# Optimization experiments

Measured on AMD Instinct MI355X. Metric: run time of the kernel, lower is better.

## Reference

```python
import jax, jax.numpy as jnp
import numpy as np

NU, NI, D, H = 200000, 100000, 128, 128
E = 600000

def _segment_mean(vals, seg_ids, num_segments):
    s = jax.ops.segment_sum(vals, seg_ids, num_segments=num_segments)
    cnt = jax.ops.segment_sum(jnp.ones((vals.shape[0],), vals.dtype), seg_ids, num_segments=num_segments)
    return s / jnp.maximum(cnt, 1.0)[:, None]


def setup_inputs() -> dict:
    key = jax.random.key(0)
    ks = jax.random.split(key, 16)
    sc = 1.0 / np.sqrt(D)
    return {
        'x_user': jax.random.normal(ks[0], (NU, D), jnp.float32),
        'x_item': jax.random.normal(ks[1], (NI, D), jnp.float32),
        'edge_src_ui': jax.random.randint(ks[2], (E,), 0, NU),
        'edge_dst_ui': jax.random.randint(ks[3], (E,), 0, NI),
        'edge_src_iu': jax.random.randint(ks[4], (E,), 0, NI),
        'edge_dst_iu': jax.random.randint(ks[5], (E,), 0, NU),
        'Wl_ui': jax.random.normal(ks[6], (D, H), jnp.float32) * sc,
        'bl_ui': jax.random.normal(ks[7], (H,), jnp.float32) * 0.01,
        'Wr_ui': jax.random.normal(ks[8], (D, H), jnp.float32) * sc,
        'Wl_iu': jax.random.normal(ks[9], (D, H), jnp.float32) * sc,
        'bl_iu': jax.random.normal(ks[10], (H,), jnp.float32) * 0.01,
        'Wr_iu': jax.random.normal(ks[11], (D, H), jnp.float32) * sc,
        'W_user': jax.random.normal(ks[12], (H, H), jnp.float32) * sc,
        'b_user': jax.random.normal(ks[13], (H,), jnp.float32) * 0.01,
        'W_item': jax.random.normal(ks[14], (H, H), jnp.float32) * sc,
        'b_item': jax.random.normal(ks[15], (H,), jnp.float32) * 0.01,
    }


def reference(x_user, x_item, edge_src_ui, edge_dst_ui, edge_src_iu, edge_dst_iu,
              Wl_ui, bl_ui, Wr_ui, Wl_iu, bl_iu, Wr_iu,
              W_user, b_user, W_item, b_item):
    # SAGEConv per edge type: out_dst = mean_aggr(x_src[src]) @ Wl + bl + x_dst @ Wr
    agg_item = _segment_mean(x_user[edge_src_ui], edge_dst_ui, NI)   # [NI, D]
    h_item = agg_item @ Wl_ui + bl_ui + x_item @ Wr_ui               # [NI, H]
    agg_user = _segment_mean(x_item[edge_src_iu], edge_dst_iu, NU)   # [NU, D]
    h_user = agg_user @ Wl_iu + bl_iu + x_user @ Wr_iu               # [NU, H]
    # HeteroConv aggr='sum' is trivial here (one edge type per dst node type).
    out_user = jax.nn.relu(h_user @ W_user + b_user)
    out_item = jax.nn.relu(h_item @ W_item + b_item)
    return jnp.concatenate([out_user, out_item], axis=0)  # [NU+NI, H]
```

## Files before the change

### kernel.cpp

```cpp
#include <hip/hip_runtime.h>

#define NUu 200000
#define NIi 100000
#define EE  600000

#define SCAP 1024
#define NB_USER 3125
#define NB_ITEM 1563

typedef short short8 __attribute__((ext_vector_type(8)));
typedef float floatx4 __attribute__((ext_vector_type(4)));

__device__ __forceinline__ unsigned short f2bf(float f) {
  union { float f; unsigned int u; } v; v.f = f;
  unsigned int r = v.u + 0x7FFFu + ((v.u >> 16) & 1u);
  return (unsigned short)(r >> 16);
}

__global__ __launch_bounds__(128) void fuse_weights(
    const float* __restrict__ Wl_iu, const float* __restrict__ Wr_iu,
    const float* __restrict__ Wl_ui, const float* __restrict__ Wr_ui,
    const float* __restrict__ W_user, const float* __restrict__ W_item,
    unsigned short* __restrict__ Wp_user, unsigned short* __restrict__ Wp_item)
{
  int d = blockIdx.x;
  int m = blockIdx.y;
  int h = threadIdx.x;
  const float* A; const float* W; unsigned short* dst; int koff;
  switch (m) {
    case 0:  A = Wl_iu; W = W_user; dst = Wp_user; koff = 0;   break;
    case 1:  A = Wr_iu; W = W_user; dst = Wp_user; koff = 128; break;
    case 2:  A = Wl_ui; W = W_item; dst = Wp_item; koff = 0;   break;
    default: A = Wr_ui; W = W_item; dst = Wp_item; koff = 128; break;
  }
  float acc = 0.f;
  for (int k = 0; k < 128; ++k) acc += A[d * 128 + k] * W[k * 128 + h];
  int kg = koff + d;
  int ks = kg >> 5, quad = (kg >> 3) & 3, j = kg & 7;
  int nt = h >> 4, nlo = h & 15;
  int idx = ((nt * 8 + ks) * 64 + quad * 16 + nlo) * 8 + j;
  dst[idx] = f2bf(acc);
}

__global__ __launch_bounds__(128) void fuse_bias(
    const float* __restrict__ bl_iu, const float* __restrict__ b_user, const float* __restrict__ Wu,
    const float* __restrict__ bl_ui, const float* __restrict__ b_item, const float* __restrict__ Wi,
    float* __restrict__ bias_user, float* __restrict__ bias_item)
{
  int h = threadIdx.x;
  const float* bl = blockIdx.x ? bl_ui : bl_iu;
  const float* b2 = blockIdx.x ? b_item : b_user;
  const float* W  = blockIdx.x ? Wi : Wu;
  float* o        = blockIdx.x ? bias_item : bias_user;
  float acc = b2[h];
  for (int k = 0; k < 128; ++k) acc += bl[k] * W[k * 128 + h];
  o[h] = acc;
}

__global__ __launch_bounds__(256) void hist2(
    const int* __restrict__ edst_iu, int* __restrict__ cnt_user,
    const int* __restrict__ edst_ui, int* __restrict__ cnt_item)
{
  int e = blockIdx.x * 256 + threadIdx.x;
  if (e >= EE) return;
  const int* edst = blockIdx.y ? edst_ui : edst_iu;
  int* cnt        = blockIdx.y ? cnt_item : cnt_user;
  atomicAdd(&cnt[edst[e]], 1);
}

__global__ __launch_bounds__(256) void scan1(
    const int* __restrict__ cnt_u, int* __restrict__ blk_u,
    const int* __restrict__ cnt_i, int* __restrict__ blk_i)
{
  __shared__ int s[256];
  int b = blockIdx.x, t = threadIdx.x;
  const int* cnt; int* blksum; int N;
  if (blockIdx.y == 0) { cnt = cnt_u; blksum = blk_u; N = NUu; }
  else { if (b >= 98) return; cnt = cnt_i; blksum = blk_i; N = NIi; }
  int base = b * 1024 + t * 4;
  int v = 0;
  #pragma unroll
  for (int j = 0; j < 4; ++j) { int i = base + j; if (i < N) v += cnt[i]; }
  s[t] = v; __syncthreads();
  for (int off = 128; off > 0; off >>= 1) {
    if (t < off) s[t] += s[t + off];
    __syncthreads();
  }
  if (t == 0) blksum[b] = s[0];
}

__global__ __launch_bounds__(256) void scan2(
    const int* __restrict__ bs_u, int* __restrict__ bo_u,
    const int* __restrict__ bs_i, int* __restrict__ bo_i)
{
  __shared__ int s[256];
  int t = threadIdx.x;
  const int* blksum = blockIdx.x ? bs_i : bs_u;
  int* blkoff       = blockIdx.x ? bo_i : bo_u;
  int nblk          = blockIdx.x ? 98 : 196;
  int v = t < nblk ? blksum[t] : 0;
  s[t] = v; __syncthreads();
  for (int off = 1; off < 256; off <<= 1) {
    int tmp = t >= off ? s[t - off] : 0;
    __syncthreads();
    s[t] += tmp;
    __syncthreads();
  }
  if (t < nblk) blkoff[t] = s[t] - v;
}

__global__ __launch_bounds__(256) void scan3(
    const int* __restrict__ cnt_u, const int* __restrict__ bo_u,
    int* __restrict__ row_u, int* __restrict__ fil_u,
    const int* __restrict__ cnt_i, const int* __restrict__ bo_i,
    int* __restrict__ row_i, int* __restrict__ fil_i)
{
  __shared__ int s[256];
  int b = blockIdx.x, t = threadIdx.x;
  const int* cnt; const int* blkoff; int* rowp; int* fillp; int N;
  if (blockIdx.y == 0) { cnt = cnt_u; blkoff = bo_u; rowp = row_u; fillp = fil_u; N = NUu; }
  else { if (b >= 98) return; cnt = cnt_i; blkoff = bo_i; rowp = row_i; fillp = fil_i; N = NIi; }
  int base = b * 1024 + t * 4;
  int v[4]; int sum = 0;
  #pragma unroll
  for (int j = 0; j < 4; ++j) { int i = base + j; v[j] = (i < N) ? cnt[i] : 0; sum += v[j]; }
  s[t] = sum; __syncthreads();
  for (int off = 1; off < 256; off <<= 1) {
    int tmp = t >= off ? s[t - off] : 0;
    __syncthreads();
    s[t] += tmp;
    __syncthreads();
  }
  int ex = s[t] - sum + blkoff[b];
  #pragma unroll
  for (int j = 0; j < 4; ++j) {
    int i = base + j;
    if (i < N) { rowp[i] = ex; fillp[i] = ex; ex += v[j]; }
  }
}

__global__ __launch_bounds__(256) void fill2(
    const int* __restrict__ esrc_iu, const int* __restrict__ edst_iu,
    int* __restrict__ fill_user, int* __restrict__ srcs_user,
    const int* __restrict__ esrc_ui, const int* __restrict__ edst_ui,
    int* __restrict__ fill_item, int* __restrict__ srcs_item)
{
  int e = blockIdx.x * 256 + threadIdx.x;
  if (e >= EE) return;
  const int* esrc; const int* edst; int* fillp; int* srcs;
  if (blockIdx.y == 0) { esrc = esrc_iu; edst = edst_iu; fillp = fill_user; srcs = srcs_user; }
  else                 { esrc = esrc_ui; edst = edst_ui; fillp = fill_item; srcs = srcs_item; }
  int d = edst[e];
  int p = atomicAdd(&fillp[d], 1);
  srcs[p] = esrc[e];
}

__global__ __launch_bounds__(256, 6) void fused_gemm(
    const float* __restrict__ xu_own, const float* __restrict__ xu_src,
    const int* __restrict__ rowp_u, const int* __restrict__ srcs_u,
    const unsigned short* __restrict__ Wp_u, const float* __restrict__ bias_u,
    const float* __restrict__ xi_own, const float* __restrict__ xi_src,
    const int* __restrict__ rowp_i, const int* __restrict__ srcs_i,
    const unsigned short* __restrict__ Wp_i, const float* __restrict__ bias_i,
    float* __restrict__ out)
{
  __shared__ __align__(16) uint4 ldsA4[1024];
  __shared__ int ldsS[SCAP];
  __shared__ int rb[65];
  int t = threadIdx.x;
  int b = blockIdx.x;

  const float* xown; const float* xsrc; const int* rowp; const int* srcs;
  const unsigned short* Wp; const float* bias; float* outbase; int nvalid; int node0;
  if (b < NB_USER) {
    xown = xu_own; xsrc = xu_src; rowp = rowp_u; srcs = srcs_u;
    Wp = Wp_u; bias = bias_u; outbase = out; nvalid = NUu; node0 = b * 64;
  } else {
    xown = xi_own; xsrc = xi_src; rowp = rowp_i; srcs = srcs_i;
    Wp = Wp_i; bias = bias_i; outbase = out + (size_t)NUu * 128;
    nvalid = NIi; node0 = (b - NB_USER) * 64;
  }

  if (t < 65) {
    int node = node0 + t;
    rb[t] = node < nvalid ? rowp[node] : EE;
  }
  __syncthreads();
  int rs0 = rb[0];
  int W = rb[64] - rs0;
  for (int idx = t; idx < W && idx < SCAP; idx += 256)
    ldsS[idx] = srcs[rs0 + idx];

  #pragma unroll
  for (int i = 0; i < 4; ++i) {
    int oid = t + i * 256;
    int m = oid >> 4;
    int oct = oid & 15;
    int node = node0 + m;
    uint4 p; p.x = 0u; p.y = 0u; p.z = 0u; p.w = 0u;
    if (node < nvalid) {
      const float4* p4 = (const float4*)(xown + (size_t)node * 128 + oct * 8);
      float4 lo = p4[0], hi = p4[1];
      p.x = (unsigned)f2bf(lo.x) | ((unsigned)f2bf(lo.y) << 16);
      p.y = (unsigned)f2bf(lo.z) | ((unsigned)f2bf(lo.w) << 16);
      p.z = (unsigned)f2bf(hi.x) | ((unsigned)f2bf(hi.y) << 16);
      p.w = (unsigned)f2bf(hi.z) | ((unsigned)f2bf(hi.w) << 16);
    }
    int ks = oct >> 2, quad = oct & 3;
    int mt = m >> 4, mlo = m & 15;
    ldsA4[(mt * 4 + ks) * 64 + quad * 16 + (mlo ^ (oct & 7))] = p;
  }
  __syncthreads();

  int wave = t >> 6, lane = t & 63;
  int quadr = lane >> 4, mlor = lane & 15;
  floatx4 acc[8];
  #pragma unroll
  for (int i = 0; i < 8; ++i) acc[i] = (floatx4){0.f, 0.f, 0.f, 0.f};
  const short8* A = (const short8*)ldsA4;
  const short8* B = (const short8*)Wp;
  #pragma unroll
  for (int kk = 0; kk < 4; ++kk) {
    short8 af = A[(wave * 4 + kk) * 64 + quadr * 16 + (mlor ^ ((kk * 4 + quadr) & 7))];
    #pragma unroll
    for (int nt = 0; nt < 8; ++nt) {
      short8 bf = B[(nt * 8 + 4 + kk) * 64 + lane];
      acc[nt] = __builtin_amdgcn_mfma_f32_16x16x32_bf16(af, bf, acc[nt], 0, 0, 0);
    }
  }
  __syncthreads();

  #pragma unroll
  for (int i = 0; i < 8; ++i) {
    int oid = t + i * 256;
    int m = oid >> 5;
    int oct = oid & 31;
    int slice = oct & 15;
    int par = oct >> 4;
    int node = node0 + m;
    float a0=0,a1=0,a2=0,a3=0,a4=0,a5=0,a6=0,a7=0;
    int deg = 0;
    if (node < nvalid) {
      int erel = rb[m] - rs0;
      deg = rb[m + 1] - rb[m];
      int k0 = slice * 8;
      int e = par;
      for (; e + 2 < deg; e += 4) {
        int q0 = erel + e, q1 = q0 + 2;
        int s0 = (q0 < SCAP) ? ldsS[q0] : srcs[rs0 + q0];
        int s1 = (q1 < SCAP) ? ldsS[q1] : srcs[rs0 + q1];
        const float4* r0 = (const float4*)(xsrc + (size_t)s0 * 128 + k0);
        const float4* r1 = (const float4*)(xsrc + (size_t)s1 * 128 + k0);
        float4 l0 = r0[0], h0 = r0[1];
        float4 l1 = r1[0], h1 = r1[1];
        a0 += l0.x + l1.x; a1 += l0.y + l1.y;
        a2 += l0.z + l1.z; a3 += l0.w + l1.w;
        a4 += h0.x + h1.x; a5 += h0.y + h1.y;
        a6 += h0.z + h1.z; a7 += h0.w + h1.w;
      }
      if (e < deg) {
        int q = erel + e;
        int s = (q < SCAP) ? ldsS[q] : srcs[rs0 + q];
        const float4* r = (const float4*)(xsrc + (size_t)s * 128 + k0);
        float4 l = r[0], h = r[1];
        a0 += l.x; a1 += l.y; a2 += l.z; a3 += l.w;
        a4 += h.x; a5 += h.y; a6 += h.z; a7 += h.w;
      }
    }
    a0 += __shfl_xor(a0, 16); a1 += __shfl_xor(a1, 16);
    a2 += __shfl_xor(a2, 16); a3 += __shfl_xor(a3, 16);
    a4 += __shfl_xor(a4, 16); a5 += __shfl_xor(a5, 16);
    a6 += __shfl_xor(a6, 16); a7 += __shfl_xor(a7, 16);
    if (par == 0) {
      float sc = deg > 0 ? 1.0f / (float)deg : 0.f;
      uint4 p;
      p.x = (unsigned)f2bf(a0 * sc) | ((unsigned)f2bf(a1 * sc) << 16);
      p.y = (unsigned)f2bf(a2 * sc) | ((unsigned)f2bf(a3 * sc) << 16);
      p.z = (unsigned)f2bf(a4 * sc) | ((unsigned)f2bf(a5 * sc) << 16);
      p.w = (unsigned)f2bf(a6 * sc) | ((unsigned)f2bf(a7 * sc) << 16);
      int ks = slice >> 2, quad = slice & 3;
      int mt = m >> 4, mlo = m & 15;
      ldsA4[(mt * 4 + ks) * 64 + quad * 16 + (mlo ^ (slice & 7))] = p;
    }
  }
  __syncthreads();

  #pragma unroll
  for (int kk = 0; kk < 4; ++kk) {
    short8 af = A[(wave * 4 + kk) * 64 + quadr * 16 + (mlor ^ ((kk * 4 + quadr) & 7))];
    #pragma unroll
    for (int nt = 0; nt < 8; ++nt) {
      short8 bf = B[(nt * 8 + kk) * 64 + lane];
      acc[nt] = __builtin_amdgcn_mfma_f32_16x16x32_bf16(af, bf, acc[nt], 0, 0, 0);
    }
  }

  int col = lane & 15, qrow = (lane >> 4) * 4;
  #pragma unroll
  for (int nt = 0; nt < 8; ++nt) {
    int n = nt * 16 + col;
    float bv = bias[n];
    #pragma unroll
    for (int r2 = 0; r2 < 4; ++r2) {
      int node = node0 + wave * 16 + qrow + r2;
      if (node < nvalid) {
        float v = acc[nt][r2] + bv;
        outbase[(size_t)node * 128 + n] = v > 0.f ? v : 0.f;
      }
    }
  }
}

extern "C" void kernel_launch(void* const* d_in, const int* in_sizes, int n_in,
                              void* d_out, int out_size, void* d_ws, size_t ws_size,
                              hipStream_t stream)
{
  const float* x_user = (const float*)d_in[0];
  const float* x_item = (const float*)d_in[1];
  const int* esrc_ui  = (const int*)d_in[2];
  const int* edst_ui  = (const int*)d_in[3];
  const int* esrc_iu  = (const int*)d_in[4];
  const int* edst_iu  = (const int*)d_in[5];
  const float* Wl_ui  = (const float*)d_in[6];
  const float* bl_ui  = (const float*)d_in[7];
  const float* Wr_ui  = (const float*)d_in[8];
  const float* Wl_iu  = (const float*)d_in[9];
  const float* bl_iu  = (const float*)d_in[10];
  const float* Wr_iu  = (const float*)d_in[11];
  const float* W_user = (const float*)d_in[12];
  const float* b_user = (const float*)d_in[13];
  const float* W_item = (const float*)d_in[14];
  const float* b_item = (const float*)d_in[15];
  float* out = (float*)d_out;

  char* ws = (char*)d_ws;
  int* cnt_user  = (int*)(ws + 0);
  int* cnt_item  = (int*)(ws + 800000);
  int* row_user  = (int*)(ws + 1200000);
  int* row_item  = (int*)(ws + 2000000);
  int* fill_user = (int*)(ws + 2400000);
  int* fill_item = (int*)(ws + 3200000);
  int* srcs_user = (int*)(ws + 3600000);
  int* srcs_item = (int*)(ws + 6000000);
  int* blks_user = (int*)(ws + 8400000);
  int* blks_item = (int*)(ws + 8401024);
  int* boff_user = (int*)(ws + 8402048);
  int* boff_item = (int*)(ws + 8403072);
  unsigned short* Wp_user = (unsigned short*)(ws + 8404224);
  unsigned short* Wp_item = (unsigned short*)(ws + 8469760);
  float* bias_user = (float*)(ws + 8535296);
  float* bias_item = (float*)(ws + 8535808);

  hipMemsetAsync(d_ws, 0, 1200000, stream);

  fuse_weights<<<dim3(128, 4), 128, 0, stream>>>(Wl_iu, Wr_iu, Wl_ui, Wr_ui,
                                                 W_user, W_item, Wp_user, Wp_item);
  fuse_bias<<<2, 128, 0, stream>>>(bl_iu, b_user, W_user, bl_ui, b_item, W_item,
                                   bias_user, bias_item);

  const int EB = (EE + 255) / 256;
  const int NBU = (NUu + 1023) / 1024;

  hist2<<<dim3(EB, 2), 256, 0, stream>>>(edst_iu, cnt_user, edst_ui, cnt_item);
  scan1<<<dim3(NBU, 2), 256, 0, stream>>>(cnt_user, blks_user, cnt_item, blks_item);
  scan2<<<2, 256, 0, stream>>>(blks_user, boff_user, blks_item, boff_item);
  scan3<<<dim3(NBU, 2), 256, 0, stream>>>(cnt_user, boff_user, row_user, fill_user,
                                          cnt_item, boff_item, row_item, fill_item);
  fill2<<<dim3(EB, 2), 256, 0, stream>>>(esrc_iu, edst_iu, fill_user, srcs_user,
                                         esrc_ui, edst_ui, fill_item, srcs_item);

  fused_gemm<<<NB_USER + NB_ITEM, 256, 0, stream>>>(
      x_user, x_item, row_user, srcs_user, Wp_user, bias_user,
      x_item, x_user, row_item, srcs_item, Wp_item, bias_item, out);
}
```

Before: 578.5 us.

## Pre-convert node features to bf16 and merge prep kernels into one launch

Adds a combined prep kernel that does the degree histogram (vectorized int4 loads), the weight and bias fusion, and a bf16 copy of x_user and x_item. The gather in fused_gemm can then read half-width rows when the workspace is large enough. The block-offset scan is folded into scan3, removing scan2. The change also raises launch bounds occupancy to 8, shrinks SCAP, and uses nontemporal output stores. The bf16 gather path lowers the precision of the aggregated sums and costs an extra full pass over the features to convert them. It only runs when ws_size is at least about 85 MB.

```diff
diff --git a/kernel.cpp b/kernel.cpp
--- a/kernel.cpp
+++ b/kernel.cpp
@@ -4,9 +4,16 @@
 #define NIi 100000
 #define EE  600000
 
-#define SCAP 1024
+#define SCAP 768
 #define NB_USER 3125
 #define NB_ITEM 1563
+
+#define PB_HIST   586
+#define PB_W0     1172
+#define PB_B0     1428
+#define PB_CU0    1429
+#define PB_CI0    13929
+#define PB_END    20179
 
 typedef short short8 __attribute__((ext_vector_type(8)));
 typedef float floatx4 __attribute__((ext_vector_type(4)));
@@ -16,56 +23,71 @@
   unsigned int r = v.u + 0x7FFFu + ((v.u >> 16) & 1u);
   return (unsigned short)(r >> 16);
 }
-
-__global__ __launch_bounds__(128) void fuse_weights(
+__device__ __forceinline__ float bflo(unsigned int u) { return __uint_as_float(u << 16); }
+__device__ __forceinline__ float bfhi(unsigned int u) { return __uint_as_float(u & 0xFFFF0000u); }
+
+__global__ __launch_bounds__(256) void prep(
+    const int* __restrict__ edst_iu, int* __restrict__ cnt_user,
+    const int* __restrict__ edst_ui, int* __restrict__ cnt_item,
     const float* __restrict__ Wl_iu, const float* __restrict__ Wr_iu,
     const float* __restrict__ Wl_ui, const float* __restrict__ Wr_ui,
     const float* __restrict__ W_user, const float* __restrict__ W_item,
-    unsigned short* __restrict__ Wp_user, unsigned short* __restrict__ Wp_item)
-{
-  int d = blockIdx.x;
-  int m = blockIdx.y;
-  int h = threadIdx.x;
-  const float* A; const float* W; unsigned short* dst; int koff;
-  switch (m) {
-    case 0:  A = Wl_iu; W = W_user; dst = Wp_user; koff = 0;   break;
-    case 1:  A = Wr_iu; W = W_user; dst = Wp_user; koff = 128; break;
-    case 2:  A = Wl_ui; W = W_item; dst = Wp_item; koff = 0;   break;
-    default: A = Wr_ui; W = W_item; dst = Wp_item; koff = 128; break;
-  }
-  float acc = 0.f;
-  for (int k = 0; k < 128; ++k) acc += A[d * 128 + k] * W[k * 128 + h];
-  int kg = koff + d;
-  int ks = kg >> 5, quad = (kg >> 3) & 3, j = kg & 7;
-  int nt = h >> 4, nlo = h & 15;
-  int idx = ((nt * 8 + ks) * 64 + quad * 16 + nlo) * 8 + j;
-  dst[idx] = f2bf(acc);
-}
-
-__global__ __launch_bounds__(128) void fuse_bias(
-    const float* __restrict__ bl_iu, const float* __restrict__ b_user, const float* __restrict__ Wu,
-    const float* __restrict__ bl_ui, const float* __restrict__ b_item, const float* __restrict__ Wi,
-    float* __restrict__ bias_user, float* __restrict__ bias_item)
-{
-  int h = threadIdx.x;
-  const float* bl = blockIdx.x ? bl_ui : bl_iu;
-  const float* b2 = blockIdx.x ? b_item : b_user;
-  const float* W  = blockIdx.x ? Wi : Wu;
-  float* o        = blockIdx.x ? bias_item : bias_user;
-  float acc = b2[h];
-  for (int k = 0; k < 128; ++k) acc += bl[k] * W[k * 128 + h];
-  o[h] = acc;
-}
-
-__global__ __launch_bounds__(256) void hist2(
-    const int* __restrict__ edst_iu, int* __restrict__ cnt_user,
-    const int* __restrict__ edst_ui, int* __restrict__ cnt_item)
-{
-  int e = blockIdx.x * 256 + threadIdx.x;
-  if (e >= EE) return;
-  const int* edst = blockIdx.y ? edst_ui : edst_iu;
-  int* cnt        = blockIdx.y ? cnt_item : cnt_user;
-  atomicAdd(&cnt[edst[e]], 1);
+    unsigned short* __restrict__ Wp_user, unsigned short* __restrict__ Wp_item,
+    const float* __restrict__ bl_iu, const float* __restrict__ b_user,
+    const float* __restrict__ bl_ui, const float* __restrict__ b_item,
+    float* __restrict__ bias_user, float* __restrict__ bias_item,
+    const float* __restrict__ x_user, const float* __restrict__ x_item,
+    unsigned short* __restrict__ xb_user, unsigned short* __restrict__ xb_item)
+{
+  int b = blockIdx.x, t = threadIdx.x;
+  if (b < PB_W0) {
+    const int* edst = b < PB_HIST ? edst_iu : edst_ui;
+    int* cnt        = b < PB_HIST ? cnt_user : cnt_item;
+    int local       = b < PB_HIST ? b : b - PB_HIST;
+    int idx = local * 1024 + t * 4;
+    if (idx < EE) {
+      int4 v = *(const int4*)(edst + idx);
+      atomicAdd(&cnt[v.x], 1); atomicAdd(&cnt[v.y], 1);
+      atomicAdd(&cnt[v.z], 1); atomicAdd(&cnt[v.w], 1);
+    }
+  } else if (b < PB_B0) {
+    int flat = (b - PB_W0) * 256 + t;
+    int h = flat & 127, d = (flat >> 7) & 127, m = flat >> 14;
+    const float* A; const float* W; unsigned short* dst; int koff;
+    switch (m) {
+      case 0:  A = Wl_iu; W = W_user; dst = Wp_user; koff = 0;   break;
+      case 1:  A = Wr_iu; W = W_user; dst = Wp_user; koff = 128; break;
+      case 2:  A = Wl_ui; W = W_item; dst = Wp_item; koff = 0;   break;
+      default: A = Wr_ui; W = W_item; dst = Wp_item; koff = 128; break;
+    }
+    float acc = 0.f;
+    for (int k = 0; k < 128; ++k) acc += A[d * 128 + k] * W[k * 128 + h];
+    int kg = koff + d;
+    int ks = kg >> 5, quad = (kg >> 3) & 3, j = kg & 7;
+    int nt = h >> 4, nlo = h & 15;
+    dst[((nt * 8 + ks) * 64 + quad * 16 + nlo) * 8 + j] = f2bf(acc);
+  } else if (b == PB_B0) {
+    int pair = t >> 7, h = t & 127;
+    const float* bl = pair ? bl_ui : bl_iu;
+    const float* b2 = pair ? b_item : b_user;
+    const float* W  = pair ? W_item : W_user;
+    float* o        = pair ? bias_item : bias_user;
+    float acc = b2[h];
+    for (int k = 0; k < 128; ++k) acc += bl[k] * W[k * 128 + h];
+    o[h] = acc;
+  } else {
+    const float* src; unsigned short* dst; long base;
+    if (b < PB_CI0) { src = x_user; dst = xb_user; base = (long)(b - PB_CU0) * 2048 + t * 8; }
+    else            { src = x_item; dst = xb_item; base = (long)(b - PB_CI0) * 2048 + t * 8; }
+    const float4* p4 = (const float4*)(src + base);
+    float4 lo = p4[0], hi = p4[1];
+    uint4 p;
+    p.x = (unsigned)f2bf(lo.x) | ((unsigned)f2bf(lo.y) << 16);
+    p.y = (unsigned)f2bf(lo.z) | ((unsigned)f2bf(lo.w) << 16);
+    p.z = (unsigned)f2bf(hi.x) | ((unsigned)f2bf(hi.y) << 16);
+    p.w = (unsigned)f2bf(hi.z) | ((unsigned)f2bf(hi.w) << 16);
+    *(uint4*)(dst + base) = p;
+  }
 }
 
 __global__ __launch_bounds__(256) void scan1(
@@ -89,37 +111,29 @@
   if (t == 0) blksum[b] = s[0];
 }
 
-__global__ __launch_bounds__(256) void scan2(
-    const int* __restrict__ bs_u, int* __restrict__ bo_u,
-    const int* __restrict__ bs_i, int* __restrict__ bo_i)
+__global__ __launch_bounds__(256) void scan3(
+    const int* __restrict__ cnt_u, const int* __restrict__ blks_u,
+    int* __restrict__ row_u, int* __restrict__ fil_u,
+    const int* __restrict__ cnt_i, const int* __restrict__ blks_i,
+    int* __restrict__ row_i, int* __restrict__ fil_i)
 {
   __shared__ int s[256];
-  int t = threadIdx.x;
-  const int* blksum = blockIdx.x ? bs_i : bs_u;
-  int* blkoff       = blockIdx.x ? bo_i : bo_u;
-  int nblk          = blockIdx.x ? 98 : 196;
-  int v = t < nblk ? blksum[t] : 0;
-  s[t] = v; __syncthreads();
+  int b = blockIdx.x, t = threadIdx.x;
+  const int* cnt; const int* blksum; int* rowp; int* fillp; int N; int nblk;
+  if (blockIdx.y == 0) { cnt = cnt_u; blksum = blks_u; rowp = row_u; fillp = fil_u; N = NUu; nblk = 196; }
+  else { if (b >= 98) return; cnt = cnt_i; blksum = blks_i; rowp = row_i; fillp = fil_i; N = NIi; nblk = 98; }
+
+  int v2 = t < nblk ? blksum[t] : 0;
+  s[t] = v2; __syncthreads();
   for (int off = 1; off < 256; off <<= 1) {
     int tmp = t >= off ? s[t - off] : 0;
     __syncthreads();
     s[t] += tmp;
     __syncthreads();
   }
-  if (t < nblk) blkoff[t] = s[t] - v;
-}
-
-__global__ __launch_bounds__(256) void scan3(
-    const int* __restrict__ cnt_u, const int* __restrict__ bo_u,
-    int* __restrict__ row_u, int* __restrict__ fil_u,
-    const int* __restrict__ cnt_i, const int* __restrict__ bo_i,
-    int* __restrict__ row_i, int* __restrict__ fil_i)
-{
-  __shared__ int s[256];
-  int b = blockIdx.x, t = threadIdx.x;
-  const int* cnt; const int* blkoff; int* rowp; int* fillp; int N;
-  if (blockIdx.y == 0) { cnt = cnt_u; blkoff = bo_u; rowp = row_u; fillp = fil_u; N = NUu; }
-  else { if (b >= 98) return; cnt = cnt_i; blkoff = bo_i; rowp = row_i; fillp = fil_i; N = NIi; }
+  int blkoffb = (b == 0) ? 0 : s[b - 1];
+  __syncthreads();
+
   int base = b * 1024 + t * 4;
   int v[4]; int sum = 0;
   #pragma unroll
@@ -131,7 +145,7 @@
     s[t] += tmp;
     __syncthreads();
   }
-  int ex = s[t] - sum + blkoff[b];
+  int ex = s[t] - sum + blkoffb;
   #pragma unroll
   for (int j = 0; j < 4; ++j) {
     int i = base + j;
@@ -155,11 +169,12 @@
   srcs[p] = esrc[e];
 }
 
-__global__ __launch_bounds__(256, 6) void fused_gemm(
-    const float* __restrict__ xu_own, const float* __restrict__ xu_src,
+template<bool BF>
+__global__ __launch_bounds__(256, 8) void fused_gemm(
+    const void* __restrict__ xu_own, const void* __restrict__ xu_src,
     const int* __restrict__ rowp_u, const int* __restrict__ srcs_u,
     const unsigned short* __restrict__ Wp_u, const float* __restrict__ bias_u,
-    const float* __restrict__ xi_own, const float* __restrict__ xi_src,
+    const void* __restrict__ xi_own, const void* __restrict__ xi_src,
     const int* __restrict__ rowp_i, const int* __restrict__ srcs_i,
     const unsigned short* __restrict__ Wp_i, const float* __restrict__ bias_i,
     float* __restrict__ out)
@@ -170,7 +185,7 @@
   int t = threadIdx.x;
   int b = blockIdx.x;
 
-  const float* xown; const float* xsrc; const int* rowp; const int* srcs;
+  const void* xown; const void* xsrc; const int* rowp; const int* srcs;
   const unsigned short* Wp; const float* bias; float* outbase; int nvalid; int node0;
   if (b < NB_USER) {
     xown = xu_own; xsrc = xu_src; rowp = rowp_u; srcs = srcs_u;
@@ -199,12 +214,16 @@
     int node = node0 + m;
     uint4 p; p.x = 0u; p.y = 0u; p.z = 0u; p.w = 0u;
     if (node < nvalid) {
-      const float4* p4 = (const float4*)(xown + (size_t)node * 128 + oct * 8);
-      float4 lo = p4[0], hi = p4[1];
-      p.x = (unsigned)f2bf(lo.x) | ((unsigned)f2bf(lo.y) << 16);
-      p.y = (unsigned)f2bf(lo.z) | ((unsigned)f2bf(lo.w) << 16);
-      p.z = (unsigned)f2bf(hi.x) | ((unsigned)f2bf(hi.y) << 16);
-      p.w = (unsigned)f2bf(hi.z) | ((unsigned)f2bf(hi.w) << 16);
+      if constexpr (BF) {
+        p = *(const uint4*)((const unsigned short*)xown + (size_t)node * 128 + oct * 8);
+      } else {
+        const float4* p4 = (const float4*)((const float*)xown + (size_t)node * 128 + oct * 8);
+        float4 lo = p4[0], hi = p4[1];
+        p.x = (unsigned)f2bf(lo.x) | ((unsigned)f2bf(lo.y) << 16);
+        p.y = (unsigned)f2bf(lo.z) | ((unsigned)f2bf(lo.w) << 16);
+        p.z = (unsigned)f2bf(hi.x) | ((unsigned)f2bf(hi.y) << 16);
+        p.w = (unsigned)f2bf(hi.z) | ((unsigned)f2bf(hi.w) << 16);
+      }
     }
     int ks = oct >> 2, quad = oct & 3;
     int mt = m >> 4, mlo = m & 15;
@@ -245,26 +264,51 @@
       deg = rb[m + 1] - rb[m];
       int k0 = slice * 8;
       int e = par;
-      for (; e + 2 < deg; e += 4) {
-        int q0 = erel + e, q1 = q0 + 2;
-        int s0 = (q0 < SCAP) ? ldsS[q0] : srcs[rs0 + q0];
-        int s1 = (q1 < SCAP) ? ldsS[q1] : srcs[rs0 + q1];
-        const float4* r0 = (const float4*)(xsrc + (size_t)s0 * 128 + k0);
-        const float4* r1 = (const float4*)(xsrc + (size_t)s1 * 128 + k0);
-        float4 l0 = r0[0], h0 = r0[1];
-        float4 l1 = r1[0], h1 = r1[1];
-        a0 += l0.x + l1.x; a1 += l0.y + l1.y;
-        a2 += l0.z + l1.z; a3 += l0.w + l1.w;
-        a4 += h0.x + h1.x; a5 += h0.y + h1.y;
-        a6 += h0.z + h1.z; a7 += h0.w + h1.w;
-      }
-      if (e < deg) {
-        int q = erel + e;
-        int s = (q < SCAP) ? ldsS[q] : srcs[rs0 + q];
-        const float4* r = (const float4*)(xsrc + (size_t)s * 128 + k0);
-        float4 l = r[0], h = r[1];
-        a0 += l.x; a1 += l.y; a2 += l.z; a3 += l.w;
-        a4 += h.x; a5 += h.y; a6 += h.z; a7 += h.w;
+      if constexpr (BF) {
+        const unsigned short* xs = (const unsigned short*)xsrc;
+        for (; e + 2 < deg; e += 4) {
+          int q0 = erel + e, q1 = q0 + 2;
+          int s0 = (q0 < SCAP) ? ldsS[q0] : srcs[rs0 + q0];
+          int s1 = (q1 < SCAP) ? ldsS[q1] : srcs[rs0 + q1];
+          uint4 v0 = *(const uint4*)(xs + (size_t)s0 * 128 + k0);
+          uint4 v1 = *(const uint4*)(xs + (size_t)s1 * 128 + k0);
+          a0 += bflo(v0.x) + bflo(v1.x); a1 += bfhi(v0.x) + bfhi(v1.x);
+          a2 += bflo(v0.y) + bflo(v1.y); a3 += bfhi(v0.y) + bfhi(v1.y);
+          a4 += bflo(v0.z) + bflo(v1.z); a5 += bfhi(v0.z) + bfhi(v1.z);
+          a6 += bflo(v0.w) + bflo(v1.w); a7 += bfhi(v0.w) + bfhi(v1.w);
+        }
+        if (e < deg) {
+          int q = erel + e;
+          int s = (q < SCAP) ? ldsS[q] : srcs[rs0 + q];
+          uint4 v0 = *(const uint4*)(xs + (size_t)s * 128 + k0);
+          a0 += bflo(v0.x); a1 += bfhi(v0.x);
+          a2 += bflo(v0.y); a3 += bfhi(v0.y);
+          a4 += bflo(v0.z); a5 += bfhi(v0.z);
+          a6 += bflo(v0.w); a7 += bfhi(v0.w);
+        }
+      } else {
+        const float* xs = (const float*)xsrc;
+        for (; e + 2 < deg; e += 4) {
+          int q0 = erel + e, q1 = q0 + 2;
+          int s0 = (q0 < SCAP) ? ldsS[q0] : srcs[rs0 + q0];
+          int s1 = (q1 < SCAP) ? ldsS[q1] : srcs[rs0 + q1];
+          const float4* r0 = (const float4*)(xs + (size_t)s0 * 128 + k0);
+          const float4* r1 = (const float4*)(xs + (size_t)s1 * 128 + k0);
+          float4 l0 = r0[0], h0 = r0[1];
+          float4 l1 = r1[0], h1 = r1[1];
+          a0 += l0.x + l1.x; a1 += l0.y + l1.y;
+          a2 += l0.z + l1.z; a3 += l0.w + l1.w;
+          a4 += h0.x + h1.x; a5 += h0.y + h1.y;
+          a6 += h0.z + h1.z; a7 += h0.w + h1.w;
+        }
+        if (e < deg) {
+          int q = erel + e;
+          int s = (q < SCAP) ? ldsS[q] : srcs[rs0 + q];
+          const float4* r = (const float4*)(xs + (size_t)s * 128 + k0);
+          float4 l = r[0], h = r[1];
+          a0 += l.x; a1 += l.y; a2 += l.z; a3 += l.w;
+          a4 += h.x; a5 += h.y; a6 += h.z; a7 += h.w;
+        }
       }
     }
     a0 += __shfl_xor(a0, 16); a1 += __shfl_xor(a1, 16);
@@ -305,7 +349,8 @@
       int node = node0 + wave * 16 + qrow + r2;
       if (node < nvalid) {
         float v = acc[nt][r2] + bv;
-        outbase[(size_t)node * 128 + n] = v > 0.f ? v : 0.f;
+        v = v > 0.f ? v : 0.f;
+        __builtin_nontemporal_store(v, &outbase[(size_t)node * 128 + n]);
       }
     }
   }
@@ -344,32 +389,38 @@
   int* srcs_item = (int*)(ws + 6000000);
   int* blks_user = (int*)(ws + 8400000);
   int* blks_item = (int*)(ws + 8401024);
-  int* boff_user = (int*)(ws + 8402048);
-  int* boff_item = (int*)(ws + 8403072);
   unsigned short* Wp_user = (unsigned short*)(ws + 8404224);
   unsigned short* Wp_item = (unsigned short*)(ws + 8469760);
   float* bias_user = (float*)(ws + 8535296);
   float* bias_item = (float*)(ws + 8535808);
+  unsigned short* xb_user = (unsigned short*)(ws + 8536320);
+  unsigned short* xb_item = (unsigned short*)(ws + 59736320UL);
+
+  const bool bf = ws_size >= 85336320UL;
 
   hipMemsetAsync(d_ws, 0, 1200000, stream);
 
-  fuse_weights<<<dim3(128, 4), 128, 0, stream>>>(Wl_iu, Wr_iu, Wl_ui, Wr_ui,
-                                                 W_user, W_item, Wp_user, Wp_item);
-  fuse_bias<<<2, 128, 0, stream>>>(bl_iu, b_user, W_user, bl_ui, b_item, W_item,
-                                   bias_user, bias_item);
+  prep<<<bf ? PB_END : PB_CU0, 256, 0, stream>>>(
+      edst_iu, cnt_user, edst_ui, cnt_item,
+      Wl_iu, Wr_iu, Wl_ui, Wr_ui, W_user, W_item, Wp_user, Wp_item,
+      bl_iu, b_user, bl_ui, b_item, bias_user, bias_item,
+      x_user, x_item, xb_user, xb_item);
+
+  scan1<<<dim3(196, 2), 256, 0, stream>>>(cnt_user, blks_user, cnt_item, blks_item);
+  scan3<<<dim3(196, 2), 256, 0, stream>>>(cnt_user, blks_user, row_user, fill_user,
+                                          cnt_item, blks_item, row_item, fill_item);
 
   const int EB = (EE + 255) / 256;
-  const int NBU = (NUu + 1023) / 1024;
-
-  hist2<<<dim3(EB, 2), 256, 0, stream>>>(edst_iu, cnt_user, edst_ui, cnt_item);
-  scan1<<<dim3(NBU, 2), 256, 0, stream>>>(cnt_user, blks_user, cnt_item, blks_item);
-  scan2<<<2, 256, 0, stream>>>(blks_user, boff_user, blks_item, boff_item);
-  scan3<<<dim3(NBU, 2), 256, 0, stream>>>(cnt_user, boff_user, row_user, fill_user,
-                                          cnt_item, boff_item, row_item, fill_item);
   fill2<<<dim3(EB, 2), 256, 0, stream>>>(esrc_iu, edst_iu, fill_user, srcs_user,
                                          esrc_ui, edst_ui, fill_item, srcs_item);
 
-  fused_gemm<<<NB_USER + NB_ITEM, 256, 0, stream>>>(
-      x_user, x_item, row_user, srcs_user, Wp_user, bias_user,
-      x_item, x_user, row_item, srcs_item, Wp_item, bias_item, out);
-}
+  if (bf) {
+    fused_gemm<true><<<NB_USER + NB_ITEM, 256, 0, stream>>>(
+        xb_user, xb_item, row_user, srcs_user, Wp_user, bias_user,
+        xb_item, xb_user, row_item, srcs_item, Wp_item, bias_item, out);
+  } else {
+    fused_gemm<false><<<NB_USER + NB_ITEM, 256, 0, stream>>>(
+        x_user, x_item, row_user, srcs_user, Wp_user, bias_user,
+        x_item, x_user, row_item, srcs_item, Wp_item, bias_item, out);
+  }
+}
```

Result: no change. 567.5 us (-1.9%).
